# Kernel tuning notes

Measured on AMD Instinct MI355X. Metric: run time of the kernel, lower is better.

Reference implementation:

```python
import jax, jax.numpy as jnp
import numpy as np

EPS = 1e-5      # F.layer_norm default eps
ALPHA = 0.08    # ALALLaDA blend coefficient


def setup_inputs() -> dict:
    key = jax.random.key(0)
    ks = jax.random.split(key, 6)
    B, S, D, K = 2, 2048, 2048, 8
    Fh = D // 4
    h_L = jax.random.normal(ks[0], (B, S, D), jnp.float32)
    # nonzero -> masked position (stands in for input_ids == 126336)
    mask = jax.random.randint(ks[1], (B, S), 0, 2).astype(jnp.int32)
    Wr = jax.random.normal(ks[2], (K, D), jnp.float32) / np.sqrt(D).astype(np.float32)
    br = jnp.zeros((K,), jnp.float32)
    W1 = jax.random.normal(ks[3], (K, D, Fh), jnp.float32) / np.sqrt(D).astype(np.float32)
    b1 = jnp.zeros((K, Fh), jnp.float32)
    W2 = jax.random.normal(ks[4], (K, Fh, D), jnp.float32) / np.sqrt(Fh).astype(np.float32)
    b2 = jnp.zeros((K, D), jnp.float32)
    return {"h_L": h_L, "mask": mask, "Wr": Wr, "br": br,
            "W1": W1, "b1": b1, "W2": W2, "b2": b2, "range_r": 8}


def _router_blend(h_L, Wr, br, W1, b1, W2, b2, mask, range_r):
    B, S, D = h_L.shape
    masked = mask != 0
    um = (~masked).astype(h_L.dtype)  # unmasked validity [B,S]
    # Per-token, per-expert outputs M[b,s,k,d]: Linear -> exact GELU -> Linear.
    pre = jnp.einsum('bsd,kdf->bskf', h_L, W1) + b1
    M = jnp.einsum('bskf,kfd->bskd', jax.nn.gelu(pre, approximate=False), W2) + b2
    # Routing weights at every position (softmax over K experts).
    w = jax.nn.softmax(jnp.einsum('bsd,kd->bsk', h_L, Wr) + br, axis=-1)
    # Accumulate weighted expert outputs over the +/-range_r neighbor window,
    # counting only unmasked neighbors. Fixed small loop over 2r offsets.
    num = jnp.zeros((B, S, D), h_L.dtype)
    cnt = jnp.zeros((B, S), h_L.dtype)
    for o in range(-range_r, range_r + 1):
        if o == 0:
            continue
        if o > 0:  # neighbor t = a + o: shift left, zero-pad tail
            Mo = jnp.pad(M[:, o:], ((0, 0), (0, o), (0, 0), (0, 0)))
            vo = jnp.pad(um[:, o:], ((0, 0), (0, o)))
        else:      # neighbor t = a + o (o<0): shift right, zero-pad head
            Mo = jnp.pad(M[:, :o], ((0, 0), (-o, 0), (0, 0), (0, 0)))
            vo = jnp.pad(um[:, :o], ((0, 0), (-o, 0)))
        num = num + vo[..., None] * jnp.einsum('bsk,bskd->bsd', w, Mo)
        cnt = cnt + vo
    has = cnt > 0
    mean = num / jnp.maximum(cnt, 1.0)[..., None]   # mean over valid neighbors
    # layer_norm over d_model, no affine
    mu = mean.mean(-1, keepdims=True)
    var = jnp.mean((mean - mu) ** 2, axis=-1, keepdims=True)
    ln = (mean - mu) / jnp.sqrt(var + EPS)
    # delta is written only at masked positions that had >=1 neighbor
    delta = jnp.where((masked & has)[..., None], ln, 0.0)
    return h_L + ALPHA * delta


def reference(h_L, mask, Wr, br, W1, b1, W2, b2, range_r):
    return _router_blend(h_L, Wr, br, W1, b1, W2, b2, mask, range_r)
```

## Files before the change

### kernel.cpp

```cpp
#include <hip/hip_runtime.h>
#include <hip/hip_bf16.h>
#include <math.h>


#define ALPHA 0.08f
#define EPS 1e-5f

typedef __attribute__((ext_vector_type(8))) __bf16 bf16x8;
typedef __attribute__((ext_vector_type(8))) short short8;
typedef __attribute__((ext_vector_type(4))) float f32x4;

__device__ __forceinline__ unsigned short f2bf(float f) {
  unsigned u = __float_as_uint(f);
  u += 0x7fffu + ((u >> 16) & 1u);
  return (unsigned short)(u >> 16);
}
__device__ __forceinline__ float bf2f(unsigned short b) {
  return __uint_as_float(((unsigned)b) << 16);
}

#define GLD16(gptr, lptr)                                                     \
  __builtin_amdgcn_global_load_lds(                                           \
      (const __attribute__((address_space(1))) void*)(gptr),                  \
      (__attribute__((address_space(3))) void*)(lptr), 16, 0, 0)

__device__ __forceinline__ int wave_incl_scan(int v, int lane) {
#pragma unroll
  for (int off = 1; off < 64; off <<= 1) {
    int t = __shfl_up(v, off);
    if (lane >= off) v += t;
  }
  return v;
}

__global__ __launch_bounds__(256) void prep_kernel(
    const float* __restrict__ h, const int* __restrict__ mask,
    const float* __restrict__ Wr, const float* __restrict__ br,
    const float* __restrict__ W1, const float* __restrict__ W2,
    const int* __restrict__ rptr, float* __restrict__ w,
    unsigned short* __restrict__ hbc, unsigned short* __restrict__ B1t,
    unsigned short* __restrict__ B2t, int* __restrict__ ru,
    int* __restrict__ msk_idx, int* __restrict__ pos2row,
    int* __restrict__ counts) {
  const int bid = blockIdx.x;
  const int tid = threadIdx.x;
  const int lane = tid & 63, wv = tid >> 6;

  if (bid < 16384) {
    __shared__ float tile[32][33];
    int id = bid;
    const float* src;
    unsigned short* dst;
    int C, c0, r0;
    size_t dstStride;
    if (id < 8192) {
      const int k = id >> 10, rem = id & 1023;
      src = W1 + (size_t)k * 2048 * 512;
      dst = B1t + (size_t)k * 512 * 2048;
      C = 512; dstStride = 2048;
      c0 = (rem >> 6) * 32; r0 = (rem & 63) * 32;
    } else {
      id -= 8192;
      const int k = id >> 10, rem = id & 1023;
      src = W2 + (size_t)k * 512 * 2048;
      dst = B2t + (size_t)k * 512;
      C = 2048; dstStride = 4096;
      c0 = (rem >> 4) * 32; r0 = (rem & 15) * 32;
    }
    const int tx = tid & 31, ty = tid >> 5;
#pragma unroll
    for (int i = 0; i < 4; ++i)
      tile[ty + 8 * i][tx] = src[(size_t)(r0 + ty + 8 * i) * C + (c0 + tx)];
    __syncthreads();
#pragma unroll
    for (int i = 0; i < 4; ++i) {
      const int c = c0 + ty + 8 * i;
      dst[(size_t)c * dstStride + (size_t)(r0 + tx)] =
          f2bf(tile[tx][ty + 8 * i]);
    }
    return;
  }

  if (bid < 20480) {
    const int a = bid - 16384;
    const size_t base = (size_t)a * 2048;
    const int d0 = tid * 8;
    float hv[8];
    *(float4*)(hv) = *(const float4*)(h + base + d0);
    *(float4*)(hv + 4) = *(const float4*)(h + base + d0 + 4);
    float acc[8];
#pragma unroll
    for (int k = 0; k < 8; ++k) {
      float wvv[8];
      *(float4*)(wvv) = *(const float4*)(Wr + (size_t)k * 2048 + d0);
      *(float4*)(wvv + 4) = *(const float4*)(Wr + (size_t)k * 2048 + d0 + 4);
      float s = 0.f;
#pragma unroll
      for (int j = 0; j < 8; ++j) s += hv[j] * wvv[j];
      acc[k] = s;
    }
    int c0n = 0;
    {
      const int4* m4p = (const int4*)mask;
#pragma unroll
      for (int q = 0; q < 4; ++q) {
        const int4 v = m4p[tid * 4 + q];
        const int b0 = tid * 16 + q * 4;
        c0n += (v.x == 0 && b0 + 0 < a);
        c0n += (v.y == 0 && b0 + 1 < a);
        c0n += (v.z == 0 && b0 + 2 < a);
        c0n += (v.w == 0 && b0 + 3 < a);
      }
    }
#pragma unroll
    for (int off = 32; off > 0; off >>= 1) {
      c0n += __shfl_down(c0n, off);
#pragma unroll
      for (int k = 0; k < 8; ++k) acc[k] += __shfl_down(acc[k], off);
    }
    __shared__ float red[4][8];
    __shared__ float logits[8];
    __shared__ int rucnt[4];
    __shared__ int rubc;
    if (lane == 0) {
#pragma unroll
      for (int k = 0; k < 8; ++k) red[wv][k] = acc[k];
      rucnt[wv] = c0n;
    }
    __syncthreads();
    if (tid < 8)
      logits[tid] =
          red[0][tid] + red[1][tid] + red[2][tid] + red[3][tid] + br[tid];
    if (tid == 0) rubc = rucnt[0] + rucnt[1] + rucnt[2] + rucnt[3];
    __syncthreads();
    if (tid == 0) {
      float mx = logits[0];
#pragma unroll
      for (int k = 1; k < 8; ++k) mx = fmaxf(mx, logits[k]);
      float e[8], se = 0.f;
#pragma unroll
      for (int k = 0; k < 8; ++k) {
        e[k] = expf(logits[k] - mx);
        se += e[k];
      }
      const float is = 1.f / se;
#pragma unroll
      for (int k = 0; k < 8; ++k) w[(size_t)a * 8 + k] = e[k] * is;
    }
    if (mask[a] == 0) {
      const int i = rubc;
      short8 o;
#pragma unroll
      for (int j = 0; j < 8; ++j) o[j] = (short)f2bf(hv[j]);
      *(short8*)(hbc + (size_t)i * 2048 + d0) = o;
    }
    return;
  }

  {
    __shared__ int sru[4097];
    __shared__ int wsum[4];
    __shared__ int wsum2[4];
    const int t0 = tid * 16;
    int mv[16];
    {
      const int4* p = (const int4*)mask;
#pragma unroll
      for (int q = 0; q < 4; ++q) {
        const int4 v = p[tid * 4 + q];
        mv[q * 4 + 0] = v.x; mv[q * 4 + 1] = v.y;
        mv[q * 4 + 2] = v.z; mv[q * 4 + 3] = v.w;
      }
    }
    int f[16];
    int c = 0;
#pragma unroll
    for (int e = 0; e < 16; ++e) { f[e] = (mv[e] == 0); c += f[e]; }
    const int isc = wave_incl_scan(c, lane);
    if (lane == 63) wsum[wv] = isc;
    __syncthreads();
    if (tid == 0) {
      int accs = 0;
#pragma unroll
      for (int i = 0; i < 4; ++i) { int v = wsum[i]; wsum[i] = accs; accs += v; }
      sru[4096] = accs;
      ru[4096] = accs;
      counts[0] = accs;
    }
    __syncthreads();
    int ex = wsum[wv] + isc - c;
#pragma unroll
    for (int e = 0; e < 16; ++e) {
      sru[t0 + e] = ex;
      ru[t0 + e] = ex;
      ex += f[e];
    }
    __syncthreads();
    const int r = rptr[0];
    int g[16];
    int c2 = 0;
#pragma unroll
    for (int e = 0; e < 16; ++e) {
      const int t = t0 + e;
      const int s = t & 2047, tb = t & ~2047;
      const int lo = max(s - r, 0), hi = min(s + r, 2047);
      const int cnt = sru[tb + hi + 1] - sru[tb + lo];
      g[e] = (mv[e] != 0 && cnt > 0) ? 1 : 0;
      c2 += g[e];
    }
    const int isc2 = wave_incl_scan(c2, lane);
    if (lane == 63) wsum2[wv] = isc2;
    __syncthreads();
    if (tid == 0) {
      int accs = 0;
#pragma unroll
      for (int i = 0; i < 4; ++i) { int v = wsum2[i]; wsum2[i] = accs; accs += v; }
      counts[1] = accs;
    }
    __syncthreads();
    int ex2 = wsum2[wv] + isc2 - c2;
#pragma unroll
    for (int e = 0; e < 16; ++e) {
      const int t = t0 + e;
      pos2row[t] = g[e] ? ex2 : -1;
      if (g[e]) msk_idx[ex2] = t;
      ex2 += g[e];
    }
  }
}

template <int EPI>
__global__ __launch_bounds__(256, 2) void gemm_bt_kernel(
    const unsigned short* __restrict__ A, const unsigned short* __restrict__ Bt,
    float* __restrict__ Cf, unsigned short* __restrict__ Cb,
    const float* __restrict__ bias, const int* __restrict__ counts, int cidx,
    int N, int Kd) {
  const int Mlim = counts[cidx];
  const int bm = blockIdx.y * 128;
  if (bm >= Mlim) return;
  __shared__ __align__(16) unsigned short L[2][16384];
  const int tid = threadIdx.x;
  const int lane = tid & 63;
  const int wid = tid >> 6;
  const int bn = blockIdx.x * 128;
  const int wr = wid >> 1;
  const int wc = wid & 1;

  f32x4 acc[4][4];
#pragma unroll
  for (int m = 0; m < 4; ++m)
#pragma unroll
    for (int n = 0; n < 4; ++n) acc[m][n] = (f32x4){0.f, 0.f, 0.f, 0.f};

  const int l8 = lane >> 3;
  const int scol = ((lane & 7) ^ l8) * 8;
  const unsigned short* gA = A + (size_t)(bm + wid * 32 + l8) * Kd + scol;
  const unsigned short* gB = Bt + (size_t)(bn + wid * 32 + l8) * Kd + scol;

  const int arow = (wr * 64 + (lane & 15)) * 64;
  const int brow = (wc * 64 + (lane & 15)) * 64;
  const int t16 = lane >> 4;
  const int x7 = lane & 7;
  const int s0 = (t16 ^ x7) * 8;
  const int s1 = ((4 + t16) ^ x7) * 8;

#define STAGE(buf, t)                                                         \
  {                                                                           \
    const int k0_ = (t) << 6;                                                 \
    unsigned short* la_ = &L[(buf)][0] + wid * 2048;                          \
    unsigned short* lb_ = &L[(buf)][8192] + wid * 2048;                       \
    GLD16(gA + k0_, la_);                                                     \
    GLD16(gA + (size_t)8 * Kd + k0_, la_ + 512);                              \
    GLD16(gA + (size_t)16 * Kd + k0_, la_ + 1024);                            \
    GLD16(gA + (size_t)24 * Kd + k0_, la_ + 1536);                            \
    GLD16(gB + k0_, lb_);                                                     \
    GLD16(gB + (size_t)8 * Kd + k0_, lb_ + 512);                              \
    GLD16(gB + (size_t)16 * Kd + k0_, lb_ + 1024);                            \
    GLD16(gB + (size_t)24 * Kd + k0_, lb_ + 1536);                            \
  }

#define COMPUTE(buf)                                                          \
  {                                                                           \
    const unsigned short* As_ = &L[(buf)][0];                                 \
    const unsigned short* Bs_ = &L[(buf)][8192];                              \
    bf16x8 a0[4], a1[4], b0[4], b1[4];                                        \
    _Pragma("unroll") for (int m = 0; m < 4; ++m) {                           \
      a0[m] = __builtin_bit_cast(bf16x8,                                      \
                                 *(const short8*)(As_ + arow + m * 1024 + s0)); \
      a1[m] = __builtin_bit_cast(bf16x8,                                      \
                                 *(const short8*)(As_ + arow + m * 1024 + s1)); \
    }                                                                         \
    _Pragma("unroll") for (int n = 0; n < 4; ++n) {                           \
      b0[n] = __builtin_bit_cast(bf16x8,                                      \
                                 *(const short8*)(Bs_ + brow + n * 1024 + s0)); \
      b1[n] = __builtin_bit_cast(bf16x8,                                      \
                                 *(const short8*)(Bs_ + brow + n * 1024 + s1)); \
    }                                                                         \
    _Pragma("unroll") for (int m = 0; m < 4; ++m)                             \
        _Pragma("unroll") for (int n = 0; n < 4; ++n) {                       \
      acc[m][n] = __builtin_amdgcn_mfma_f32_16x16x32_bf16(a0[m], b0[n],       \
                                                          acc[m][n], 0, 0, 0); \
      acc[m][n] = __builtin_amdgcn_mfma_f32_16x16x32_bf16(a1[m], b1[n],       \
                                                          acc[m][n], 0, 0, 0); \
    }                                                                         \
  }

  const int nt = Kd >> 6;
  STAGE(0, 0);
  STAGE(1, 1);
#pragma unroll 1
  for (int t = 0; t < nt - 2; ++t) {
    asm volatile("s_waitcnt vmcnt(8)" ::: "memory");
    __builtin_amdgcn_s_barrier();
    __builtin_amdgcn_sched_barrier(0);
    COMPUTE(t & 1);
    __builtin_amdgcn_s_barrier();
    STAGE(t & 1, t + 2);
  }
  asm volatile("s_waitcnt vmcnt(8)" ::: "memory");
  __builtin_amdgcn_s_barrier();
  __builtin_amdgcn_sched_barrier(0);
  COMPUTE(nt & 1);
  asm volatile("s_waitcnt vmcnt(0)" ::: "memory");
  __builtin_amdgcn_s_barrier();
  __builtin_amdgcn_sched_barrier(0);
  COMPUTE((nt - 1) & 1);
#undef STAGE
#undef COMPUTE

  const int r0 = bm + wr * 64 + (lane >> 4) * 4;
  const int c0 = bn + wc * 64 + (lane & 15);
#pragma unroll
  for (int m = 0; m < 4; ++m) {
#pragma unroll
    for (int n = 0; n < 4; ++n) {
      const int col = c0 + n * 16;
#pragma unroll
      for (int i = 0; i < 4; ++i) {
        const int row = r0 + m * 16 + i;
        if (row >= Mlim) continue;
        const size_t off = (size_t)row * N + col;
        float v = acc[m][n][i];
        if (EPI == 1) {
          v += bias[col];
          v = 0.5f * v * (1.0f + erff(v * 0.70710678118654752f));
          Cb[off] = f2bf(v);
        } else {
          Cf[off] = v;
        }
      }
    }
  }
}

__global__ void window_kernel(const unsigned short* __restrict__ Act_c,
                              const float* __restrict__ w,
                              const int* __restrict__ msk_idx,
                              const int* __restrict__ ru,
                              const int* __restrict__ rptr,
                              const int* __restrict__ counts,
                              unsigned short* __restrict__ G_c) {
  const int Nm = counts[1];
  const int o = blockIdx.y;
  const int q = (Nm + 7) >> 3;
  const int y = o >> 3;
  if (y >= q) return;
  const int i = (o & 7) * q + y;
  if (i >= Nm) return;
  const int a = msk_idx[i];
  const int s = a & 2047;
  const int tb = a & ~2047;
  const int r = rptr[0];
  const int lo = max(s - r, 0), hi = min(s + r, 2047);
  const int jlo = ru[tb + lo], jhi = ru[tb + hi + 1];
  const int c = blockIdx.x * 2048 + threadIdx.x * 8;
  float acc[8] = {0.f, 0.f, 0.f, 0.f, 0.f, 0.f, 0.f, 0.f};
  for (int j = jlo; j < jhi; ++j) {
    const short8 v = *(const short8*)(Act_c + (size_t)j * 4096 + c);
#pragma unroll
    for (int jj = 0; jj < 8; ++jj) acc[jj] += bf2f((unsigned short)v[jj]);
  }
  const float wv = w[(size_t)a * 8 + (c >> 9)];
  short8 o8;
#pragma unroll
  for (int jj = 0; jj < 8; ++jj) o8[jj] = (short)f2bf(acc[jj] * wv);
  *(short8*)(G_c + (size_t)i * 4096 + c) = o8;
}

__global__ void final_kernel(const float* __restrict__ h,
                             const int* __restrict__ pos2row,
                             const float* __restrict__ w,
                             const float* __restrict__ b2,
                             const float* __restrict__ num_c,
                             const int* __restrict__ ru,
                             const int* __restrict__ rptr,
                             float* __restrict__ out) {
  const int a = blockIdx.x;
  const int tid = threadIdx.x;
  const int lane = tid & 63, wid = tid >> 6;
  const size_t base = (size_t)a * 2048;
  const int d0 = tid * 8;
  const int row = pos2row[a];
  if (row < 0) {
    const float4 x0 = *(const float4*)(h + base + d0);
    const float4 x1 = *(const float4*)(h + base + d0 + 4);
    *(float4*)(out + base + d0) = x0;
    *(float4*)(out + base + d0 + 4) = x1;
    return;
  }
  const int s = a & 2047;
  const int tb = a & ~2047;
  const int r = rptr[0];
  const int lo = max(s - r, 0), hi = min(s + r, 2047);
  const int cnt = ru[tb + hi + 1] - ru[tb + lo];
  float wk[8];
#pragma unroll
  for (int k = 0; k < 8; ++k) wk[k] = w[(size_t)a * 8 + k];
  const float cntf = (float)cnt;
  const float icnt = 1.0f / cntf;
  float mval[8];
  float s1 = 0.f, s2 = 0.f;
#pragma unroll
  for (int j = 0; j < 8; ++j) {
    const int d = d0 + j;
    float wb2 = 0.f;
#pragma unroll
    for (int k = 0; k < 8; ++k) wb2 += wk[k] * b2[(size_t)k * 2048 + d];
    const float v = (num_c[(size_t)row * 2048 + d] + cntf * wb2) * icnt;
    mval[j] = v;
    s1 += v;
    s2 += v * v;
  }
#pragma unroll
  for (int off = 32; off > 0; off >>= 1) {
    s1 += __shfl_down(s1, off);
    s2 += __shfl_down(s2, off);
  }
  __shared__ float red[8];
  if (lane == 0) {
    red[wid] = s1;
    red[4 + wid] = s2;
  }
  __syncthreads();
  const float S1 = red[0] + red[1] + red[2] + red[3];
  const float S2 = red[4] + red[5] + red[6] + red[7];
  const float mu = S1 * (1.0f / 2048.0f);
  const float var = S2 * (1.0f / 2048.0f) - mu * mu;
  const float rin = rsqrtf(var + EPS);
#pragma unroll
  for (int j = 0; j < 8; ++j) {
    const int d = d0 + j;
    out[base + d] = h[base + d] + ALPHA * ((mval[j] - mu) * rin);
  }
}

extern "C" void kernel_launch(void* const* d_in, const int* in_sizes, int n_in,
                              void* d_out, int out_size, void* d_ws,
                              size_t ws_size, hipStream_t stream) {
  const float* h = (const float*)d_in[0];
  const int* mask = (const int*)d_in[1];
  const float* Wr = (const float*)d_in[2];
  const float* br = (const float*)d_in[3];
  const float* W1 = (const float*)d_in[4];
  const float* b1 = (const float*)d_in[5];
  const float* W2 = (const float*)d_in[6];
  const float* b2 = (const float*)d_in[7];
  const int* rptr = (const int*)d_in[8];
  float* out = (float*)d_out;

  char* ws = (char*)d_ws;
  unsigned short* hbc = (unsigned short*)(ws + 0);
  unsigned short* B1t = (unsigned short*)(ws + 16777216);
  unsigned short* B2t = (unsigned short*)(ws + 33554432);
  unsigned short* Act_c = (unsigned short*)(ws + 50331648);
  unsigned short* G_c = (unsigned short*)(ws + 83886080);
  float* num_c = (float*)(ws + 50331648);
  float* wbuf = (float*)(ws + 117440512);
  int* ru = (int*)(ws + 117571584);
  int* msk_idx = ru + 4100;
  int* pos2row = msk_idx + 4096;
  int* counts = pos2row + 4096;

  prep_kernel<<<20481, 256, 0, stream>>>(h, mask, Wr, br, W1, W2, rptr, wbuf,
                                         hbc, B1t, B2t, ru, msk_idx, pos2row,
                                         counts);
  gemm_bt_kernel<1><<<dim3(32, 32), 256, 0, stream>>>(
      hbc, B1t, nullptr, Act_c, b1, counts, 0, 4096, 2048);
  window_kernel<<<dim3(2, 4096), 256, 0, stream>>>(Act_c, wbuf, msk_idx, ru,
                                                   rptr, counts, G_c);
  gemm_bt_kernel<0><<<dim3(16, 32), 256, 0, stream>>>(
      G_c, B2t, num_c, nullptr, nullptr, counts, 1, 2048, 4096);
  final_kernel<<<4096, 256, 0, stream>>>(h, pos2row, wbuf, b2, num_c, ru,
                                         rptr, out);
}
```

Before: 308.5 us.

## Make GEMMs persistent with 256-row tiles, triple-buffered LDS and XCD-aware tile mapping

```diff
diff --git a/kernel.cpp b/kernel.cpp
--- a/kernel.cpp
+++ b/kernel.cpp
@@ -23,6 +23,8 @@
   __builtin_amdgcn_global_load_lds(                                           \
       (const __attribute__((address_space(1))) void*)(gptr),                  \
       (__attribute__((address_space(3))) void*)(lptr), 16, 0, 0)
+
+#define LD8(p) __builtin_bit_cast(bf16x8, *(const short8*)(p))
 
 __device__ __forceinline__ int wave_incl_scan(int v, int lane) {
 #pragma unroll
@@ -229,75 +231,73 @@
   }
 }
 
-template <int EPI>
-__global__ __launch_bounds__(256, 2) void gemm_bt_kernel(
+template <int EPI, int BNW>
+__global__ __launch_bounds__(512, 2) void gemm_bt_kernel(
     const unsigned short* __restrict__ A, const unsigned short* __restrict__ Bt,
     float* __restrict__ Cf, unsigned short* __restrict__ Cb,
     const float* __restrict__ bias, const int* __restrict__ counts, int cidx,
     int N, int Kd) {
-  const int Mlim = counts[cidx];
-  const int bm = blockIdx.y * 128;
-  if (bm >= Mlim) return;
-  __shared__ __align__(16) unsigned short L[2][16384];
+  constexpr int BIW = BNW / 64;
+  constexpr int NF = BNW / 32;
+  constexpr int SBUF = 16384 + BNW * 64;
+  __shared__ __align__(16) unsigned short L[3 * SBUF];
   const int tid = threadIdx.x;
   const int lane = tid & 63;
   const int wid = tid >> 6;
-  const int bn = blockIdx.x * 128;
   const int wr = wid >> 1;
   const int wc = wid & 1;
-
-  f32x4 acc[4][4];
-#pragma unroll
-  for (int m = 0; m < 4; ++m)
-#pragma unroll
-    for (int n = 0; n < 4; ++n) acc[m][n] = (f32x4){0.f, 0.f, 0.f, 0.f};
-
   const int l8 = lane >> 3;
-  const int scol = ((lane & 7) ^ l8) * 8;
-  const unsigned short* gA = A + (size_t)(bm + wid * 32 + l8) * Kd + scol;
-  const unsigned short* gB = Bt + (size_t)(bn + wid * 32 + l8) * Kd + scol;
+  const int sc = ((lane & 7) ^ l8) * 8;
+
+  const int Mlim = counts[cidx];
+  const int nbm = (Mlim + 255) >> 8;
+  const int nbn = N / BNW;
+  const int ntiles = nbm * nbn;
+  const int ntpx = (ntiles + 7) >> 3;
+  const int xcd = blockIdx.x & 7;
+  const int slot = blockIdx.x >> 3;
 
   const int arow = (wr * 64 + (lane & 15)) * 64;
-  const int brow = (wc * 64 + (lane & 15)) * 64;
+  const int brow = 16384 + (wc * (BNW / 2) + (lane & 15)) * 64;
   const int t16 = lane >> 4;
   const int x7 = lane & 7;
   const int s0 = (t16 ^ x7) * 8;
   const int s1 = ((4 + t16) ^ x7) * 8;
+  const int nt = Kd >> 6;
+
+#define VMWAIT_P                                                              \
+  do {                                                                        \
+    if (BIW == 2) asm volatile("s_waitcnt vmcnt(6)" ::: "memory");            \
+    else asm volatile("s_waitcnt vmcnt(5)" ::: "memory");                     \
+  } while (0)
 
 #define STAGE(buf, t)                                                         \
   {                                                                           \
-    const int k0_ = (t) << 6;                                                 \
-    unsigned short* la_ = &L[(buf)][0] + wid * 2048;                          \
-    unsigned short* lb_ = &L[(buf)][8192] + wid * 2048;                       \
+    const size_t k0_ = (size_t)(t) << 6;                                      \
+    unsigned short* la_ = L + (buf) * SBUF + wid * 2048;                      \
+    unsigned short* lb_ = L + (buf) * SBUF + 16384 + wid * (512 * BIW);       \
     GLD16(gA + k0_, la_);                                                     \
     GLD16(gA + (size_t)8 * Kd + k0_, la_ + 512);                              \
     GLD16(gA + (size_t)16 * Kd + k0_, la_ + 1024);                            \
     GLD16(gA + (size_t)24 * Kd + k0_, la_ + 1536);                            \
     GLD16(gB + k0_, lb_);                                                     \
-    GLD16(gB + (size_t)8 * Kd + k0_, lb_ + 512);                              \
-    GLD16(gB + (size_t)16 * Kd + k0_, lb_ + 1024);                            \
-    GLD16(gB + (size_t)24 * Kd + k0_, lb_ + 1536);                            \
+    if (BIW == 2) GLD16(gB + (size_t)8 * Kd + k0_, lb_ + 512);                \
   }
 
 #define COMPUTE(buf)                                                          \
   {                                                                           \
-    const unsigned short* As_ = &L[(buf)][0];                                 \
-    const unsigned short* Bs_ = &L[(buf)][8192];                              \
-    bf16x8 a0[4], a1[4], b0[4], b1[4];                                        \
+    const unsigned short* bb_ = L + (buf) * SBUF;                             \
+    bf16x8 a0[4], a1[4], b0[NF], b1[NF];                                      \
     _Pragma("unroll") for (int m = 0; m < 4; ++m) {                           \
-      a0[m] = __builtin_bit_cast(bf16x8,                                      \
-                                 *(const short8*)(As_ + arow + m * 1024 + s0)); \
-      a1[m] = __builtin_bit_cast(bf16x8,                                      \
-                                 *(const short8*)(As_ + arow + m * 1024 + s1)); \
+      a0[m] = LD8(bb_ + arow + m * 1024 + s0);                                \
+      a1[m] = LD8(bb_ + arow + m * 1024 + s1);                                \
     }                                                                         \
-    _Pragma("unroll") for (int n = 0; n < 4; ++n) {                           \
-      b0[n] = __builtin_bit_cast(bf16x8,                                      \
-                                 *(const short8*)(Bs_ + brow + n * 1024 + s0)); \
-      b1[n] = __builtin_bit_cast(bf16x8,                                      \
-                                 *(const short8*)(Bs_ + brow + n * 1024 + s1)); \
+    _Pragma("unroll") for (int n = 0; n < NF; ++n) {                          \
+      b0[n] = LD8(bb_ + brow + n * 1024 + s0);                                \
+      b1[n] = LD8(bb_ + brow + n * 1024 + s1);                                \
     }                                                                         \
     _Pragma("unroll") for (int m = 0; m < 4; ++m)                             \
-        _Pragma("unroll") for (int n = 0; n < 4; ++n) {                       \
+        _Pragma("unroll") for (int n = 0; n < NF; ++n) {                      \
       acc[m][n] = __builtin_amdgcn_mfma_f32_16x16x32_bf16(a0[m], b0[n],       \
                                                           acc[m][n], 0, 0, 0); \
       acc[m][n] = __builtin_amdgcn_mfma_f32_16x16x32_bf16(a1[m], b1[n],       \
@@ -305,52 +305,73 @@
     }                                                                         \
   }
 
-  const int nt = Kd >> 6;
-  STAGE(0, 0);
-  STAGE(1, 1);
 #pragma unroll 1
-  for (int t = 0; t < nt - 2; ++t) {
-    asm volatile("s_waitcnt vmcnt(8)" ::: "memory");
+  for (int i = slot; i < ntpx; i += 32) {
+    const int tau = xcd * ntpx + i;
+    if (tau >= ntiles) break;
+    const int bn = (tau / nbm) * BNW;
+    const int bm = (tau % nbm) * 256;
+
+    f32x4 acc[4][NF];
+#pragma unroll
+    for (int m = 0; m < 4; ++m)
+#pragma unroll
+      for (int n = 0; n < NF; ++n) acc[m][n] = (f32x4){0.f, 0.f, 0.f, 0.f};
+
+    const unsigned short* gA = A + (size_t)(bm + wid * 32 + l8) * Kd + sc;
+    const unsigned short* gB = Bt + (size_t)(bn + wid * 8 * BIW + l8) * Kd + sc;
+
+    STAGE(0, 0);
+    STAGE(1, 1);
+    int cb = 0, sb = 2;
+#pragma unroll 1
+    for (int t = 0; t < nt - 2; ++t) {
+      VMWAIT_P;
+      __builtin_amdgcn_s_barrier();
+      __builtin_amdgcn_sched_barrier(0);
+      STAGE(sb, t + 2);
+      COMPUTE(cb);
+      cb = (cb == 2) ? 0 : cb + 1;
+      sb = (sb == 2) ? 0 : sb + 1;
+    }
+    VMWAIT_P;
     __builtin_amdgcn_s_barrier();
     __builtin_amdgcn_sched_barrier(0);
-    COMPUTE(t & 1);
+    COMPUTE(cb);
+    cb = (cb == 2) ? 0 : cb + 1;
+    asm volatile("s_waitcnt vmcnt(0)" ::: "memory");
     __builtin_amdgcn_s_barrier();
-    STAGE(t & 1, t + 2);
-  }
-  asm volatile("s_waitcnt vmcnt(8)" ::: "memory");
-  __builtin_amdgcn_s_barrier();
-  __builtin_amdgcn_sched_barrier(0);
-  COMPUTE(nt & 1);
-  asm volatile("s_waitcnt vmcnt(0)" ::: "memory");
-  __builtin_amdgcn_s_barrier();
-  __builtin_amdgcn_sched_barrier(0);
-  COMPUTE((nt - 1) & 1);
+    __builtin_amdgcn_sched_barrier(0);
+    COMPUTE(cb);
+
+    const int r0 = bm + wr * 64 + (lane >> 4) * 4;
+    const int c0 = bn + wc * (BNW / 2) + (lane & 15);
+#pragma unroll
+    for (int m = 0; m < 4; ++m) {
+#pragma unroll
+      for (int n = 0; n < NF; ++n) {
+        const int col = c0 + n * 16;
+#pragma unroll
+        for (int ii = 0; ii < 4; ++ii) {
+          const int row = r0 + m * 16 + ii;
+          if (row >= Mlim) continue;
+          const size_t off = (size_t)row * N + col;
+          float v = acc[m][n][ii];
+          if (EPI == 1) {
+            v += bias[col];
+            v = 0.5f * v * (1.0f + erff(v * 0.70710678118654752f));
+            Cb[off] = f2bf(v);
+          } else {
+            Cf[off] = v;
+          }
+        }
+      }
+    }
+    __builtin_amdgcn_s_barrier();
+  }
 #undef STAGE
 #undef COMPUTE
-
-  const int r0 = bm + wr * 64 + (lane >> 4) * 4;
-  const int c0 = bn + wc * 64 + (lane & 15);
-#pragma unroll
-  for (int m = 0; m < 4; ++m) {
-#pragma unroll
-    for (int n = 0; n < 4; ++n) {
-      const int col = c0 + n * 16;
-#pragma unroll
-      for (int i = 0; i < 4; ++i) {
-        const int row = r0 + m * 16 + i;
-        if (row >= Mlim) continue;
-        const size_t off = (size_t)row * N + col;
-        float v = acc[m][n][i];
-        if (EPI == 1) {
-          v += bias[col];
-          v = 0.5f * v * (1.0f + erff(v * 0.70710678118654752f));
-          Cb[off] = f2bf(v);
-        } else {
-          Cf[off] = v;
-        }
-      }
-    }
-  }
+#undef VMWAIT_P
 }
 
 __global__ void window_kernel(const unsigned short* __restrict__ Act_c,
@@ -484,12 +505,13 @@
   prep_kernel<<<20481, 256, 0, stream>>>(h, mask, Wr, br, W1, W2, rptr, wbuf,
                                          hbc, B1t, B2t, ru, msk_idx, pos2row,
                                          counts);
-  gemm_bt_kernel<1><<<dim3(32, 32), 256, 0, stream>>>(
-      hbc, B1t, nullptr, Act_c, b1, counts, 0, 4096, 2048);
+  gemm_bt_kernel<1, 128><<<256, 512, 0, stream>>>(hbc, B1t, nullptr, Act_c,
+                                                  b1, counts, 0, 4096, 2048);
   window_kernel<<<dim3(2, 4096), 256, 0, stream>>>(Act_c, wbuf, msk_idx, ru,
                                                    rptr, counts, G_c);
-  gemm_bt_kernel<0><<<dim3(16, 32), 256, 0, stream>>>(
-      G_c, B2t, num_c, nullptr, nullptr, counts, 1, 2048, 4096);
+  gemm_bt_kernel<0, 64><<<256, 512, 0, stream>>>(G_c, B2t, num_c, nullptr,
+                                                 nullptr, counts, 1, 2048,
+                                                 4096);
   final_kernel<<<4096, 256, 0, stream>>>(h, pos2row, wbuf, b2, num_c, ru,
                                          rptr, out);
 }
```

Result: slower. 327.2 us (+6.1%).
